# Optimization experiments

Hardware: AMD Instinct MI355X
Metric: run time of the kernel (lower is better)

## Reference

```python
import jax, jax.numpy as jnp
import numpy as np

NUM_EXPERTS = 8
TOP_K = 2


def setup_inputs() -> dict:
    key = jax.random.key(0)
    ks = jax.random.split(key, 6)
    B, S, D, H, E = 4, 1024, 1024, 2048, NUM_EXPERTS
    x = jax.random.normal(ks[0], (B, S, D), dtype=jnp.float32)
    Wg = jax.random.normal(ks[1], (D, E), dtype=jnp.float32) * 0.02
    W1 = jax.random.normal(ks[2], (E, D, H), dtype=jnp.float32) * 0.02
    b1 = jax.random.normal(ks[3], (E, H), dtype=jnp.float32) * 0.02
    W2 = jax.random.normal(ks[4], (E, H, D), dtype=jnp.float32) * 0.02
    b2 = jax.random.normal(ks[5], (E, D), dtype=jnp.float32) * 0.02
    return {"x": x, "Wg": Wg, "W1": W1, "b1": b1, "W2": W2, "b2": b2}


def reference(x, Wg, W1, b1, W2, b2):
    B, S, D = x.shape
    E, _, H = W1.shape
    OUT = W2.shape[2]
    xm = x.reshape(-1, D)                      # [N, D], N = B*S
    # --- top-k gating (ProbabilitySamplerTopk): softmax over experts, take top-k ---
    logits = xm @ Wg                           # [N, E]
    probs = jax.nn.softmax(logits, axis=-1)
    topk_p, topk_i = jax.lax.top_k(probs, TOP_K)   # [N, K]
    # --- sort dispatched (token, expert) pairs by expert id (stable) ---
    flat_e = topk_i.reshape(-1)                # [N*K]
    flat_p = topk_p.reshape(-1)                # [N*K]
    order = jnp.argsort(flat_e)                # stable sort -> grouped by expert
    tok_idx = order // TOP_K                   # source token index (trunc-div by topK)
    e_sorted = flat_e[order]                   # [N*K]
    p_sorted = flat_p[order]                   # [N*K]
    xs = xm[tok_idx]                           # [N*K, D] expert-sorted inputs
    # --- grouped-GEMM experts: masked per-expert dense GEMM (E is small & fixed) ---
    y = jnp.zeros((xs.shape[0], OUT), dtype=xs.dtype)
    for e in range(E):
        h = jax.nn.relu(xs @ W1[e] + b1[e])    # [N*K, H]
        ye = h @ W2[e] + b2[e]                 # [N*K, OUT]
        m = (e_sorted == e)[:, None].astype(xs.dtype)
        y = y + m * ye
    # --- combine: multiply by gates, scatter-add back to token slots ---
    y = y * p_sorted[:, None]
    out = jnp.zeros((B * S, OUT), dtype=y.dtype).at[tok_idx].add(y)
    return out.reshape(B, S, OUT)
```

## Files before the change

### kernel.cpp

```cpp
#include <hip/hip_runtime.h>
#include <hip/hip_bf16.h>
#include <stdint.h>

typedef __bf16 bf16;
typedef __bf16 bf16x8 __attribute__((ext_vector_type(8)));
typedef __bf16 bf16x4 __attribute__((ext_vector_type(4)));
typedef float f32x4 __attribute__((ext_vector_type(4)));

#define N_TOK 4096
#define DDIM 1024
#define HDIM 2048
#define NPAIR 8192
#define BMT 256
#define MTILES 39

__device__ __forceinline__ void gload16(const void* g, void* l) {
  __builtin_amdgcn_global_load_lds(
      (const __attribute__((address_space(1))) unsigned int*)g,
      (__attribute__((address_space(3))) unsigned int*)l, 16, 0, 0);
}

__global__ void cvt_x_kernel(const float* __restrict__ x, bf16* __restrict__ xb) {
  int i = (blockIdx.x * 256 + threadIdx.x) * 8;
  float4 a = *(const float4*)(x + i);
  float4 b = *(const float4*)(x + i + 4);
  bf16x8 o = {(bf16)a.x, (bf16)a.y, (bf16)a.z, (bf16)a.w,
              (bf16)b.x, (bf16)b.y, (bf16)b.z, (bf16)b.w};
  *(bf16x8*)(xb + i) = o;
}

__global__ void transpose_cvt_kernel(const float* __restrict__ in, bf16* __restrict__ out,
                                     int R, int C) {
  __shared__ float tile[32][33];
  const float* ip = in + (size_t)blockIdx.z * R * C;
  bf16* op = out + (size_t)blockIdx.z * R * C;
  int r0 = blockIdx.y * 32, c0 = blockIdx.x * 32;
  int tr = threadIdx.x >> 3;
  int tc = (threadIdx.x & 7) * 4;
  float4 v = *(const float4*)(ip + (size_t)(r0 + tr) * C + c0 + tc);
  tile[tr][tc] = v.x; tile[tr][tc + 1] = v.y; tile[tr][tc + 2] = v.z; tile[tr][tc + 3] = v.w;
  __syncthreads();
  bf16x4 o = {(bf16)tile[tc + 0][tr], (bf16)tile[tc + 1][tr],
              (bf16)tile[tc + 2][tr], (bf16)tile[tc + 3][tr]};
  *(bf16x4*)(op + (size_t)(c0 + tr) * R + r0 + tc) = o;
}

__global__ void gate_kernel(const float* __restrict__ x, const float* __restrict__ Wg,
                            int2* __restrict__ ge, float2* __restrict__ gp) {
  int t = blockIdx.x * 4 + (threadIdx.x >> 6);
  int lane = threadIdx.x & 63;
  const float* xr = x + (size_t)t * DDIM;
  float a[8];
#pragma unroll
  for (int e = 0; e < 8; e++) a[e] = 0.f;
  for (int d = lane; d < DDIM; d += 64) {
    float xv = xr[d];
    float4 w0 = *(const float4*)(Wg + d * 8);
    float4 w1 = *(const float4*)(Wg + d * 8 + 4);
    a[0] += xv * w0.x; a[1] += xv * w0.y; a[2] += xv * w0.z; a[3] += xv * w0.w;
    a[4] += xv * w1.x; a[5] += xv * w1.y; a[6] += xv * w1.z; a[7] += xv * w1.w;
  }
#pragma unroll
  for (int off = 32; off >= 1; off >>= 1) {
#pragma unroll
    for (int e = 0; e < 8; e++) a[e] += __shfl_xor(a[e], off);
  }
  if (lane == 0) {
    float m = a[0];
#pragma unroll
    for (int e = 1; e < 8; e++) m = fmaxf(m, a[e]);
    float p[8]; float s = 0.f;
#pragma unroll
    for (int e = 0; e < 8; e++) { p[e] = expf(a[e] - m); s += p[e]; }
    float inv = 1.f / s;
    int i0 = 0; float v0 = a[0];
#pragma unroll
    for (int e = 1; e < 8; e++) if (a[e] > v0) { v0 = a[e]; i0 = e; }
    int i1 = -1; float v1 = -1e30f;
#pragma unroll
    for (int e = 0; e < 8; e++) if (e != i0 && a[e] > v1) { v1 = a[e]; i1 = e; }
    ge[t] = make_int2(i0, i1);
    gp[t] = make_float2(p[i0] * inv, p[i1] * inv);
  }
}

__global__ void sort_kernel(const int2* __restrict__ ge, const float2* __restrict__ gp,
                            int* __restrict__ tok, float* __restrict__ ps,
                            int* __restrict__ pairpos, int* __restrict__ meta) {
  __shared__ int hist[8], runn[8], wc[16][8], wb[16][8], baseS[9];
  int tid = threadIdx.x;
  int lane = tid & 63, wv = tid >> 6;
  if (tid < 8) hist[tid] = 0;
  __syncthreads();
  for (int i = tid; i < NPAIR; i += 1024) {
    int2 g = ge[i >> 1];
    int e = (i & 1) ? g.y : g.x;
    atomicAdd(&hist[e], 1);
  }
  __syncthreads();
  if (tid == 0) {
    int b = 0, ts = 0;
    for (int e = 0; e < 8; e++) {
      baseS[e] = b; meta[e] = b; meta[9 + e] = ts;
      b += hist[e]; ts += (hist[e] + BMT - 1) / BMT;
    }
    baseS[8] = b; meta[8] = b; meta[17] = ts;
  }
  __syncthreads();
  if (tid < 8) runn[tid] = baseS[tid];
  __syncthreads();
  for (int c = 0; c < 8; c++) {
    int i = c * 1024 + tid;
    int2 g = ge[i >> 1];
    int e = (i & 1) ? g.y : g.x;
    int rank = 0;
#pragma unroll
    for (int ee = 0; ee < 8; ee++) {
      unsigned long long b = __ballot(e == ee);
      if (e == ee) rank = __popcll(b & ((1ull << lane) - 1ull));
      if (lane == 0) wc[wv][ee] = __popcll(b);
    }
    __syncthreads();
    if (tid < 8) {
      int s = runn[tid];
      for (int w = 0; w < 16; w++) { wb[w][tid] = s; s += wc[w][tid]; }
      runn[tid] = s;
    }
    __syncthreads();
    int pos = wb[wv][e] + rank;
    tok[pos] = i >> 1;
    float2 p2 = gp[i >> 1];
    ps[pos] = (i & 1) ? p2.y : p2.x;
    pairpos[i] = pos;
    __syncthreads();
  }
}

template <int KDIM, int NPE, bool FIRST>
__global__ __launch_bounds__(512, 2)
void moe_gemm_kernel(const bf16* __restrict__ A, const bf16* __restrict__ Bt,
                     const float* __restrict__ bias, const int* __restrict__ tok,
                     const float* __restrict__ ps, const int* __restrict__ meta,
                     bf16* __restrict__ hout, float* __restrict__ y2, int MT) {
  __shared__ bf16 lds[3][24576];

  int nwg = gridDim.x;
  int orig = blockIdx.x;
  int q = nwg >> 3, rr8 = nwg & 7;
  int xcd = orig & 7, off8 = orig >> 3;
  int lin = (xcd < rr8 ? xcd * (q + 1) : rr8 * (q + 1) + (xcd - rr8) * q) + off8;
  int tileN = lin / MT;
  int tileM = lin - tileN * MT;
  if (tileM >= meta[17]) return;
  int e = 0;
#pragma unroll
  for (int k = 1; k < 8; k++) if (tileM >= meta[9 + k]) e = k;
  int row0 = meta[e] + (tileM - meta[9 + e]) * BMT;
  int segEnd = meta[e + 1];
  int n0 = tileN * 128;

  int t = threadIdx.x;
  const bf16* aSrc[4];
  const bf16* bSrc[2];
#pragma unroll
  for (int r = 0; r < 4; r++) {
    int row = r * 64 + (t >> 3);
    int gRow = row0 + row; if (gRow > NPAIR - 1) gRow = NPAIR - 1;
    int arow = FIRST ? tok[gRow] : gRow;
    int gcol = ((t & 7) ^ (row & 7)) * 8;
    aSrc[r] = A + (size_t)arow * KDIM + gcol;
  }
#pragma unroll
  for (int r = 0; r < 2; r++) {
    int row = r * 64 + (t >> 3);
    int gcol = ((t & 7) ^ (row & 7)) * 8;
    bSrc[r] = Bt + ((size_t)e * NPE + n0 + row) * KDIM + gcol;
  }

  int lane = t & 63, wv = t >> 6;
  int wm = wv >> 1, wn = wv & 1;
  int l15 = lane & 15, l4 = lane >> 4;
  int aOff[4], bOff[4];
#pragma unroll
  for (int m = 0; m < 4; m++) {
    int row = wm * 64 + m * 16 + l15;
    aOff[m] = row * 64 + ((l4 ^ (row & 7)) * 8);
  }
#pragma unroll
  for (int n = 0; n < 4; n++) {
    int row = wn * 64 + n * 16 + l15;
    bOff[n] = 16384 + row * 64 + ((l4 ^ (row & 7)) * 8);
  }

  f32x4 acc[4][4];
#pragma unroll
  for (int m = 0; m < 4; m++)
#pragma unroll
    for (int n = 0; n < 4; n++)
#pragma unroll
      for (int j = 0; j < 4; j++) acc[m][n][j] = 0.f;

  auto STAGE = [&](int kt, int slot) {
    bf16* sb = &lds[slot][0];
    int ko = kt * 64;
    gload16(aSrc[0] + ko, sb + t * 8);
    gload16(aSrc[1] + ko, sb + 4096 + t * 8);
    gload16(aSrc[2] + ko, sb + 8192 + t * 8);
    gload16(aSrc[3] + ko, sb + 12288 + t * 8);
    gload16(bSrc[0] + ko, sb + 16384 + t * 8);
    gload16(bSrc[1] + ko, sb + 20480 + t * 8);
  };

  constexpr int nk = KDIM / 64;
  STAGE(0, 0);
  STAGE(1, 1);
  for (int kt = 0; kt < nk; kt++) {
    if (kt == nk - 1) asm volatile("s_waitcnt vmcnt(0)\n\ts_barrier" ::: "memory");
    else              asm volatile("s_waitcnt vmcnt(6)\n\ts_barrier" ::: "memory");
    if (kt + 2 < nk) STAGE(kt + 2, (kt + 2) % 3);
    __builtin_amdgcn_sched_barrier(0);
    const bf16* sb = &lds[kt % 3][0];
#pragma unroll
    for (int ks = 0; ks < 2; ks++) {
      bf16x8 af[4], bfr[4];
#pragma unroll
      for (int m = 0; m < 4; m++) af[m] = *(const bf16x8*)(sb + (aOff[m] ^ (ks << 5)));
#pragma unroll
      for (int n = 0; n < 4; n++) bfr[n] = *(const bf16x8*)(sb + (bOff[n] ^ (ks << 5)));
      __builtin_amdgcn_s_setprio(1);
#pragma unroll
      for (int m = 0; m < 4; m++)
#pragma unroll
        for (int n = 0; n < 4; n++)
          acc[m][n] = __builtin_amdgcn_mfma_f32_16x16x32_bf16(af[m], bfr[n], acc[m][n], 0, 0, 0);
      __builtin_amdgcn_s_setprio(0);
    }
  }

  int colb = n0 + wn * 64 + l15;
  int rowb = wm * 64 + l4 * 4;
  float bia[4];
#pragma unroll
  for (int n = 0; n < 4; n++) bia[n] = bias[(size_t)e * NPE + colb + n * 16];
#pragma unroll
  for (int m = 0; m < 4; m++) {
#pragma unroll
    for (int j = 0; j < 4; j++) {
      int gRow = row0 + rowb + m * 16 + j;
      if (gRow < segEnd) {
        if (FIRST) {
#pragma unroll
          for (int n = 0; n < 4; n++) {
            float v = acc[m][n][j] + bia[n];
            v = fmaxf(v, 0.f);
            hout[(size_t)gRow * NPE + colb + n * 16] = (bf16)v;
          }
        } else {
          float pscale = ps[gRow];
#pragma unroll
          for (int n = 0; n < 4; n++) {
            float v = (acc[m][n][j] + bia[n]) * pscale;
            y2[(size_t)gRow * NPE + colb + n * 16] = v;
          }
        }
      }
    }
  }
}

__global__ void combine_kernel(const float* __restrict__ y2, const int* __restrict__ pairpos,
                               float* __restrict__ out) {
  int gi = blockIdx.x * 256 + threadIdx.x;
  int tk = gi >> 8;
  int c4 = (gi & 255) * 4;
  int p0 = pairpos[tk * 2], p1 = pairpos[tk * 2 + 1];
  float4 a = *(const float4*)(y2 + (size_t)p0 * DDIM + c4);
  float4 b = *(const float4*)(y2 + (size_t)p1 * DDIM + c4);
  float4 o = {a.x + b.x, a.y + b.y, a.z + b.z, a.w + b.w};
  *(float4*)(out + (size_t)tk * DDIM + c4) = o;
}

extern "C" void kernel_launch(void* const* d_in, const int* in_sizes, int n_in,
                              void* d_out, int out_size, void* d_ws, size_t ws_size,
                              hipStream_t stream) {
  (void)in_sizes; (void)n_in; (void)out_size; (void)ws_size;
  const float* x  = (const float*)d_in[0];
  const float* Wg = (const float*)d_in[1];
  const float* W1 = (const float*)d_in[2];
  const float* b1 = (const float*)d_in[3];
  const float* W2 = (const float*)d_in[4];
  const float* b2 = (const float*)d_in[5];
  float* out = (float*)d_out;

  char* ws = (char*)d_ws;
  bf16*  xb   = (bf16*)(ws);
  bf16*  W1T  = (bf16*)(ws + (8ull  << 20));
  bf16*  W2T  = (bf16*)(ws + (40ull << 20));
  bf16*  hbuf = (bf16*)(ws + (72ull << 20));
  float* y2   = (float*)(ws + (104ull << 20));
  char*  ext  = ws + (136ull << 20);
  int2*   ge      = (int2*)(ext);
  float2* gp      = (float2*)(ext + (64u  << 10));
  int*    tok     = (int*)(ext + (128u << 10));
  float*  psarr   = (float*)(ext + (160u << 10));
  int*    pairpos = (int*)(ext + (192u << 10));
  int*    meta    = (int*)(ext + (224u << 10));

  cvt_x_kernel<<<2048, 256, 0, stream>>>(x, xb);
  transpose_cvt_kernel<<<dim3(64, 32, 8), 256, 0, stream>>>(W1, W1T, 1024, 2048);
  transpose_cvt_kernel<<<dim3(32, 64, 8), 256, 0, stream>>>(W2, W2T, 2048, 1024);
  gate_kernel<<<1024, 256, 0, stream>>>(x, Wg, ge, gp);
  sort_kernel<<<1, 1024, 0, stream>>>(ge, gp, tok, psarr, pairpos, meta);
  moe_gemm_kernel<1024, 2048, true><<<dim3(MTILES * 16), 512, 0, stream>>>(
      xb, W1T, b1, tok, psarr, meta, hbuf, nullptr, MTILES);
  moe_gemm_kernel<2048, 1024, false><<<dim3(MTILES * 8), 512, 0, stream>>>(
      hbuf, W2T, b2, tok, psarr, meta, nullptr, y2, MTILES);
  combine_kernel<<<4096, 256, 0, stream>>>(y2, pairpos, out);
}
```

Measured before the change: 212.8 us.

## Shrink MoE GEMM tiles to 128x128x32 with 256 threads and fuse x conversion into gating

The grouped GEMM moves from 256x128 tiles with BK=64 and 512 threads to 128x128 tiles with BK=32 and 256 threads. This cuts padding waste per expert segment and raises the number of workgroups and occupancy (launch bounds 256,3), at the cost of less operand reuse per tile and more barriers per K step. The LDS swizzle is adapted to the 32-wide K rows. Separately, the fp32-to-bf16 conversion of x is folded into the gate kernel, which now reads x as float4, removing one kernel launch and one full pass over x.

```diff
diff --git a/kernel.cpp b/kernel.cpp
--- a/kernel.cpp
+++ b/kernel.cpp
@@ -11,22 +11,15 @@
 #define DDIM 1024
 #define HDIM 2048
 #define NPAIR 8192
-#define BMT 256
-#define MTILES 39
+#define BM 128
+#define BN 128
+#define BK 32
+#define MTILES 71
 
 __device__ __forceinline__ void gload16(const void* g, void* l) {
   __builtin_amdgcn_global_load_lds(
       (const __attribute__((address_space(1))) unsigned int*)g,
       (__attribute__((address_space(3))) unsigned int*)l, 16, 0, 0);
-}
-
-__global__ void cvt_x_kernel(const float* __restrict__ x, bf16* __restrict__ xb) {
-  int i = (blockIdx.x * 256 + threadIdx.x) * 8;
-  float4 a = *(const float4*)(x + i);
-  float4 b = *(const float4*)(x + i + 4);
-  bf16x8 o = {(bf16)a.x, (bf16)a.y, (bf16)a.z, (bf16)a.w,
-              (bf16)b.x, (bf16)b.y, (bf16)b.z, (bf16)b.w};
-  *(bf16x8*)(xb + i) = o;
 }
 
 __global__ void transpose_cvt_kernel(const float* __restrict__ in, bf16* __restrict__ out,
@@ -46,19 +39,29 @@
 }
 
 __global__ void gate_kernel(const float* __restrict__ x, const float* __restrict__ Wg,
-                            int2* __restrict__ ge, float2* __restrict__ gp) {
+                            int2* __restrict__ ge, float2* __restrict__ gp,
+                            bf16* __restrict__ xb) {
   int t = blockIdx.x * 4 + (threadIdx.x >> 6);
   int lane = threadIdx.x & 63;
   const float* xr = x + (size_t)t * DDIM;
+  bf16* xbr = xb + (size_t)t * DDIM;
   float a[8];
 #pragma unroll
   for (int e = 0; e < 8; e++) a[e] = 0.f;
-  for (int d = lane; d < DDIM; d += 64) {
-    float xv = xr[d];
-    float4 w0 = *(const float4*)(Wg + d * 8);
-    float4 w1 = *(const float4*)(Wg + d * 8 + 4);
-    a[0] += xv * w0.x; a[1] += xv * w0.y; a[2] += xv * w0.z; a[3] += xv * w0.w;
-    a[4] += xv * w1.x; a[5] += xv * w1.y; a[6] += xv * w1.z; a[7] += xv * w1.w;
+#pragma unroll
+  for (int it = 0; it < 4; it++) {
+    int d0 = it * 256 + lane * 4;
+    float4 xv = *(const float4*)(xr + d0);
+    bf16x4 o = {(bf16)xv.x, (bf16)xv.y, (bf16)xv.z, (bf16)xv.w};
+    *(bf16x4*)(xbr + d0) = o;
+    float xs[4] = {xv.x, xv.y, xv.z, xv.w};
+#pragma unroll
+    for (int dd = 0; dd < 4; dd++) {
+      float4 w0 = *(const float4*)(Wg + (size_t)(d0 + dd) * 8);
+      float4 w1 = *(const float4*)(Wg + (size_t)(d0 + dd) * 8 + 4);
+      a[0] += xs[dd] * w0.x; a[1] += xs[dd] * w0.y; a[2] += xs[dd] * w0.z; a[3] += xs[dd] * w0.w;
+      a[4] += xs[dd] * w1.x; a[5] += xs[dd] * w1.y; a[6] += xs[dd] * w1.z; a[7] += xs[dd] * w1.w;
+    }
   }
 #pragma unroll
   for (int off = 32; off >= 1; off >>= 1) {
@@ -102,7 +105,7 @@
     int b = 0, ts = 0;
     for (int e = 0; e < 8; e++) {
       baseS[e] = b; meta[e] = b; meta[9 + e] = ts;
-      b += hist[e]; ts += (hist[e] + BMT - 1) / BMT;
+      b += hist[e]; ts += (hist[e] + BM - 1) / BM;
     }
     baseS[8] = b; meta[8] = b; meta[17] = ts;
   }
@@ -137,12 +140,12 @@
 }
 
 template <int KDIM, int NPE, bool FIRST>
-__global__ __launch_bounds__(512, 2)
+__global__ __launch_bounds__(256, 3)
 void moe_gemm_kernel(const bf16* __restrict__ A, const bf16* __restrict__ Bt,
                      const float* __restrict__ bias, const int* __restrict__ tok,
                      const float* __restrict__ ps, const int* __restrict__ meta,
                      bf16* __restrict__ hout, float* __restrict__ y2, int MT) {
-  __shared__ bf16 lds[3][24576];
+  __shared__ bf16 lds[3][8192];
 
   int nwg = gridDim.x;
   int orig = blockIdx.x;
@@ -155,25 +158,20 @@
   int e = 0;
 #pragma unroll
   for (int k = 1; k < 8; k++) if (tileM >= meta[9 + k]) e = k;
-  int row0 = meta[e] + (tileM - meta[9 + e]) * BMT;
+  int row0 = meta[e] + (tileM - meta[9 + e]) * BM;
   int segEnd = meta[e + 1];
-  int n0 = tileN * 128;
+  int n0 = tileN * BN;
 
   int t = threadIdx.x;
-  const bf16* aSrc[4];
+  const bf16* aSrc[2];
   const bf16* bSrc[2];
 #pragma unroll
-  for (int r = 0; r < 4; r++) {
-    int row = r * 64 + (t >> 3);
+  for (int r = 0; r < 2; r++) {
+    int row = r * 64 + (t >> 2);
     int gRow = row0 + row; if (gRow > NPAIR - 1) gRow = NPAIR - 1;
     int arow = FIRST ? tok[gRow] : gRow;
-    int gcol = ((t & 7) ^ (row & 7)) * 8;
+    int gcol = ((t & 3) ^ ((row >> 1) & 3)) * 8;
     aSrc[r] = A + (size_t)arow * KDIM + gcol;
-  }
-#pragma unroll
-  for (int r = 0; r < 2; r++) {
-    int row = r * 64 + (t >> 3);
-    int gcol = ((t & 7) ^ (row & 7)) * 8;
     bSrc[r] = Bt + ((size_t)e * NPE + n0 + row) * KDIM + gcol;
   }
 
@@ -184,12 +182,12 @@
 #pragma unroll
   for (int m = 0; m < 4; m++) {
     int row = wm * 64 + m * 16 + l15;
-    aOff[m] = row * 64 + ((l4 ^ (row & 7)) * 8);
+    aOff[m] = row * 32 + ((l4 ^ ((row >> 1) & 3)) * 8);
   }
 #pragma unroll
   for (int n = 0; n < 4; n++) {
     int row = wn * 64 + n * 16 + l15;
-    bOff[n] = 16384 + row * 64 + ((l4 ^ (row & 7)) * 8);
+    bOff[n] = 4096 + row * 32 + ((l4 ^ ((row >> 1) & 3)) * 8);
   }
 
   f32x4 acc[4][4];
@@ -202,39 +200,34 @@
 
   auto STAGE = [&](int kt, int slot) {
     bf16* sb = &lds[slot][0];
-    int ko = kt * 64;
+    int ko = kt * BK;
     gload16(aSrc[0] + ko, sb + t * 8);
-    gload16(aSrc[1] + ko, sb + 4096 + t * 8);
-    gload16(aSrc[2] + ko, sb + 8192 + t * 8);
-    gload16(aSrc[3] + ko, sb + 12288 + t * 8);
-    gload16(bSrc[0] + ko, sb + 16384 + t * 8);
-    gload16(bSrc[1] + ko, sb + 20480 + t * 8);
+    gload16(aSrc[1] + ko, sb + 2048 + t * 8);
+    gload16(bSrc[0] + ko, sb + 4096 + t * 8);
+    gload16(bSrc[1] + ko, sb + 6144 + t * 8);
   };
 
-  constexpr int nk = KDIM / 64;
+  constexpr int nk = KDIM / BK;
   STAGE(0, 0);
   STAGE(1, 1);
   for (int kt = 0; kt < nk; kt++) {
     if (kt == nk - 1) asm volatile("s_waitcnt vmcnt(0)\n\ts_barrier" ::: "memory");
-    else              asm volatile("s_waitcnt vmcnt(6)\n\ts_barrier" ::: "memory");
+    else              asm volatile("s_waitcnt vmcnt(4)\n\ts_barrier" ::: "memory");
     if (kt + 2 < nk) STAGE(kt + 2, (kt + 2) % 3);
     __builtin_amdgcn_sched_barrier(0);
     const bf16* sb = &lds[kt % 3][0];
-#pragma unroll
-    for (int ks = 0; ks < 2; ks++) {
-      bf16x8 af[4], bfr[4];
-#pragma unroll
-      for (int m = 0; m < 4; m++) af[m] = *(const bf16x8*)(sb + (aOff[m] ^ (ks << 5)));
-#pragma unroll
-      for (int n = 0; n < 4; n++) bfr[n] = *(const bf16x8*)(sb + (bOff[n] ^ (ks << 5)));
-      __builtin_amdgcn_s_setprio(1);
-#pragma unroll
-      for (int m = 0; m < 4; m++)
-#pragma unroll
-        for (int n = 0; n < 4; n++)
-          acc[m][n] = __builtin_amdgcn_mfma_f32_16x16x32_bf16(af[m], bfr[n], acc[m][n], 0, 0, 0);
-      __builtin_amdgcn_s_setprio(0);
-    }
+    bf16x8 af[4], bfr[4];
+#pragma unroll
+    for (int m = 0; m < 4; m++) af[m] = *(const bf16x8*)(sb + aOff[m]);
+#pragma unroll
+    for (int n = 0; n < 4; n++) bfr[n] = *(const bf16x8*)(sb + bOff[n]);
+    __builtin_amdgcn_s_setprio(1);
+#pragma unroll
+    for (int m = 0; m < 4; m++)
+#pragma unroll
+      for (int n = 0; n < 4; n++)
+        acc[m][n] = __builtin_amdgcn_mfma_f32_16x16x32_bf16(af[m], bfr[n], acc[m][n], 0, 0, 0);
+    __builtin_amdgcn_s_setprio(0);
   }
 
   int colb = n0 + wn * 64 + l15;
@@ -306,14 +299,13 @@
   int*    pairpos = (int*)(ext + (192u << 10));
   int*    meta    = (int*)(ext + (224u << 10));
 
-  cvt_x_kernel<<<2048, 256, 0, stream>>>(x, xb);
   transpose_cvt_kernel<<<dim3(64, 32, 8), 256, 0, stream>>>(W1, W1T, 1024, 2048);
   transpose_cvt_kernel<<<dim3(32, 64, 8), 256, 0, stream>>>(W2, W2T, 2048, 1024);
-  gate_kernel<<<1024, 256, 0, stream>>>(x, Wg, ge, gp);
+  gate_kernel<<<1024, 256, 0, stream>>>(x, Wg, ge, gp, xb);
   sort_kernel<<<1, 1024, 0, stream>>>(ge, gp, tok, psarr, pairpos, meta);
-  moe_gemm_kernel<1024, 2048, true><<<dim3(MTILES * 16), 512, 0, stream>>>(
+  moe_gemm_kernel<1024, 2048, true><<<dim3(MTILES * 16), 256, 0, stream>>>(
       xb, W1T, b1, tok, psarr, meta, hbuf, nullptr, MTILES);
-  moe_gemm_kernel<2048, 1024, false><<<dim3(MTILES * 8), 512, 0, stream>>>(
+  moe_gemm_kernel<2048, 1024, false><<<dim3(MTILES * 8), 256, 0, stream>>>(
       hbuf, W2T, b2, tok, psarr, meta, nullptr, y2, MTILES);
   combine_kernel<<<4096, 256, 0, stream>>>(y2, pairpos, out);
 }
```

Result: no change. 208.8 us (-1.9%).
